# Kernel tuning notes

Measured on AMD Instinct MI355X. Metric: run time of the kernel, lower is better.

The kernel has to match this reference:

```python
import jax, jax.numpy as jnp
import numpy as np

B, L, D = 4, 2048, 1024
E, F, H = 6, 1536, 512  # experts, d_ff, router hidden
TOP_K = 2
LN_EPS = 1e-5

def setup_inputs() -> dict:
    key = jax.random.key(0)
    ks = jax.random.split(key, 8)
    s = lambda fan: 1.0 / np.sqrt(fan)
    return {
        "x": jax.random.normal(ks[0], (B, L, D), jnp.float32),
        "r1_w": jax.random.normal(ks[1], (D, H), jnp.float32) * s(D),
        "r1_b": jnp.zeros((H,), jnp.float32),
        "ln_g": jnp.ones((H,), jnp.float32),
        "ln_b": jnp.zeros((H,), jnp.float32),
        "r2_w": jax.random.normal(ks[2], (H, E), jnp.float32) * s(H),
        "r2_b": jnp.zeros((E,), jnp.float32),
        "temp": jnp.ones((1,), jnp.float32),
        "route_bias": jnp.zeros((E,), jnp.float32),
        "W1": jax.random.normal(ks[3], (E, D, F), jnp.float32) * s(D),
        "b1": jnp.zeros((E, F), jnp.float32),
        "W2": jax.random.normal(ks[4], (E, F, D), jnp.float32) * s(F),
        "b2": jnp.zeros((E, D), jnp.float32),
    }

def reference(x, r1_w, r1_b, ln_g, ln_b, r2_w, r2_b, temp, route_bias, W1, b1, W2, b2):
    b, l, d = x.shape
    xf = x.reshape(-1, d)                       # [N, D]
    n = xf.shape[0]
    # Router: Linear -> LayerNorm -> GELU(exact) -> Linear
    h = xf @ r1_w + r1_b                        # [N, H]
    mu = jnp.mean(h, axis=-1, keepdims=True)
    var = jnp.mean((h - mu) ** 2, axis=-1, keepdims=True)
    h = (h - mu) * jax.lax.rsqrt(var + LN_EPS) * ln_g + ln_b
    h = jax.nn.gelu(h, approximate=False)
    logits = (h @ r2_w + r2_b) / temp + route_bias   # [N, E]
    p = jax.nn.softmax(logits, axis=-1)
    top_v, top_i = jax.lax.top_k(p, TOP_K)      # [N, k]
    probs = jnp.zeros_like(p).at[jnp.arange(n)[:, None], top_i].set(top_v)  # [N, E]
    # Dense all-expert MLPs (faithful to source, which computes every expert)
    hh = jnp.einsum('nd,edf->enf', xf, W1) + b1[:, None, :]   # [E, N, F]
    even = (jnp.arange(W1.shape[0]) % 2 == 0)[:, None, None]
    act = jnp.where(even, jax.nn.gelu(hh, approximate=False), jax.nn.silu(hh))
    eo = jnp.einsum('enf,efd->end', act, W2) + b2[:, None, :]  # [E, N, D]
    out = jnp.einsum('ne,end->nd', probs, eo)   # weighted combine
    return out.reshape(b, l, d)
```

## Files before the change

kernel.cpp:

```cpp
#include <hip/hip_runtime.h>
#include <hip/hip_bf16.h>
#include <stdint.h>

typedef __bf16 bf16;
typedef bf16 bf16x8 __attribute__((ext_vector_type(8)));
typedef bf16 bf16x4 __attribute__((ext_vector_type(4)));
typedef float f32x4 __attribute__((ext_vector_type(4)));
typedef int i32x4 __attribute__((ext_vector_type(4)));

#define N_TOK 8192
#define D_MODEL 1024
#define H_R 512
#define N_EXP 6
#define F_FF 1536
#define FLAG_CAP 1024

__device__ __forceinline__ float erf_fast(float x) {
    float ax = fabsf(x);
    float t = 1.0f / (1.0f + 0.3275911f * ax);
    float p = t * (0.254829592f + t * (-0.284496736f + t * (1.421413741f +
              t * (-1.453152027f + t * 1.061405429f))));
    float r = 1.0f - p * __expf(-ax * ax);
    return copysignf(r, x);
}
__device__ __forceinline__ float gelu_f(float x) {
    return 0.5f * x * (1.0f + erf_fast(x * 0.70710678118654752f));
}
__device__ __forceinline__ float silu_f(float x) {
    return x * (1.0f / (1.0f + __expf(-x)));
}

typedef __attribute__((address_space(1))) const void* gas1;
typedef __attribute__((address_space(3))) void* las3;

__device__ __forceinline__ void gload16(const void* g, void* l) {
    __builtin_amdgcn_global_load_lds((gas1)g, (las3)l, 16, 0, 0);
}

__device__ __forceinline__ int swz_src_q(int c) {
    return (((c & 3) - ((c >> 2) >> 1)) & 3);
}

#define GATE(N) asm volatile("s_waitcnt vmcnt(" #N ")\n\ts_barrier" ::: "memory")


__global__ __launch_bounds__(256) void convert_x_split(
    const float* __restrict__ x, bf16* __restrict__ xh, bf16* __restrict__ xl) {
    size_t i = ((size_t)blockIdx.x * 256 + threadIdx.x) * 8;
    f32x4 a = *(const f32x4*)(x + i);
    f32x4 b = *(const f32x4*)(x + i + 4);
    float v[8] = {a[0], a[1], a[2], a[3], b[0], b[1], b[2], b[3]};
    bf16x8 vh, vl;
    #pragma unroll
    for (int k = 0; k < 8; ++k) {
        bf16 h = (bf16)v[k];
        vh[k] = h;
        vl[k] = (bf16)(v[k] - (float)h);
    }
    *(bf16x8*)(xh + i) = vh;
    *(bf16x8*)(xl + i) = vl;
}

__global__ __launch_bounds__(256) void transpose_bf16_64(
    const float* __restrict__ in, bf16* __restrict__ out, int R, int C) {
    __shared__ float tile[64][65];
    const float* inp = in + (size_t)blockIdx.z * R * C;
    bf16* op = out + (size_t)blockIdx.z * R * C;
    int tx = threadIdx.x & 15, ty = threadIdx.x >> 4;
    int r0 = blockIdx.y * 64, c0 = blockIdx.x * 64;
    #pragma unroll
    for (int p = 0; p < 4; ++p) {
        int row = p * 16 + ty;
        f32x4 v = *(const f32x4*)(inp + (size_t)(r0 + row) * C + c0 + tx * 4);
        tile[row][tx * 4 + 0] = v[0];
        tile[row][tx * 4 + 1] = v[1];
        tile[row][tx * 4 + 2] = v[2];
        tile[row][tx * 4 + 3] = v[3];
    }
    __syncthreads();
    #pragma unroll
    for (int p = 0; p < 4; ++p) {
        int cc = p * 16 + ty;
        bf16x4 o;
        #pragma unroll
        for (int k = 0; k < 4; ++k) o[k] = (bf16)tile[tx * 4 + k][cc];
        *(bf16x4*)(op + (size_t)(c0 + cc) * R + r0 + tx * 4) = o;
    }
}

__global__ __launch_bounds__(256) void transpose_split(
    const float* __restrict__ in, bf16* __restrict__ oh, bf16* __restrict__ ol,
    int R, int C) {
    __shared__ float tile[32][33];
    int tx = threadIdx.x & 31, ty = threadIdx.x >> 5;
    int r0 = blockIdx.y * 32, c0 = blockIdx.x * 32;
    #pragma unroll
    for (int yy = ty; yy < 32; yy += 8)
        tile[yy][tx] = in[(size_t)(r0 + yy) * C + c0 + tx];
    __syncthreads();
    #pragma unroll
    for (int yy = ty; yy < 32; yy += 8) {
        float v = tile[tx][yy];
        bf16 h = (bf16)v;
        size_t o = (size_t)(c0 + yy) * R + r0 + tx;
        oh[o] = h;
        ol[o] = (bf16)(v - (float)h);
    }
}


__device__ __forceinline__ void gemm128_core(
    const bf16* gA0, const bf16* gA1, const bf16* gB0, const bf16* gB1,
    int K, bf16* sm, f32x4 acc[4][4])
{
    const int tid = threadIdx.x;
    const int lane = tid & 63;
    const int w = tid >> 6;
    const int wm = w & 1, wn = w >> 1;
    const int lc = lane & 15;
    const int koff = ((((lane >> 4) + (lc >> 1)) & 3) * 8);
    gload16(gA0, sm + w * 512);
    gload16(gA1, sm + 2048 + w * 512);
    gload16(gB0, sm + 4096 + w * 512);
    gload16(gB1, sm + 6144 + w * 512);
    int bo = 0;
    const int NT = K >> 5;
    for (int t = 0; t < NT; ++t) {
        const int nb = bo ^ 8192;
        if (t + 1 < NT) {
            const int kb = (t + 1) << 5;
            gload16(gA0 + kb, sm + nb + w * 512);
            gload16(gA1 + kb, sm + nb + 2048 + w * 512);
            gload16(gB0 + kb, sm + nb + 4096 + w * 512);
            gload16(gB1 + kb, sm + nb + 6144 + w * 512);
            GATE(4);
        } else {
            GATE(0);
        }
        bf16x8 af[4], bfr[4];
        #pragma unroll
        for (int i = 0; i < 4; ++i)
            af[i] = *(const bf16x8*)(sm + bo + (wm * 64 + i * 16 + lc) * 32 + koff);
        #pragma unroll
        for (int j = 0; j < 4; ++j)
            bfr[j] = *(const bf16x8*)(sm + bo + 4096 + (wn * 64 + j * 16 + lc) * 32 + koff);
        __builtin_amdgcn_s_barrier();
        __builtin_amdgcn_s_setprio(1);
        #pragma unroll
        for (int i = 0; i < 4; ++i)
            #pragma unroll
            for (int j = 0; j < 4; ++j)
                acc[i][j] = __builtin_amdgcn_mfma_f32_16x16x32_bf16(af[i], bfr[j], acc[i][j], 0, 0, 0);
        __builtin_amdgcn_s_setprio(0);
        bo = nb;
    }
}


__global__ __launch_bounds__(256, 2) void router_gemm_fused(
    const bf16* __restrict__ xh, const bf16* __restrict__ xl,
    const bf16* __restrict__ wTh, const bf16* __restrict__ wTl,
    float* __restrict__ hp) {
    __shared__ bf16 smem[32768];
    const int tid = threadIdx.x;
    const int mbase = blockIdx.y * 128, nbase = blockIdx.x * 128;
    const int c0 = tid, c1 = tid + 256;
    const size_t ra0 = (size_t)(mbase + (c0 >> 2)) * D_MODEL + swz_src_q(c0) * 8;
    const size_t ra1 = (size_t)(mbase + (c1 >> 2)) * D_MODEL + swz_src_q(c1) * 8;
    const size_t rb0 = (size_t)(nbase + (c0 >> 2)) * D_MODEL + swz_src_q(c0) * 8;
    const size_t rb1 = (size_t)(nbase + (c1 >> 2)) * D_MODEL + swz_src_q(c1) * 8;
    const bf16 *pxh0 = xh + ra0, *pxh1 = xh + ra1;
    const bf16 *pxl0 = xl + ra0, *pxl1 = xl + ra1;
    const bf16 *pwh0 = wTh + rb0, *pwh1 = wTh + rb1;
    const bf16 *pwl0 = wTl + rb0, *pwl1 = wTl + rb1;
    const int w = tid >> 6, lane = tid & 63;
    const int wm = w & 1, wn = w >> 1, lc = lane & 15;
    const int koff = ((((lane >> 4) + (lc >> 1)) & 3) * 8);
    const int ws = w * 512;
    f32x4 acc[4][4] = {};
    gload16(pxh0, smem + ws);
    gload16(pxh1, smem + 2048 + ws);
    gload16(pxl0, smem + 4096 + ws);
    gload16(pxl1, smem + 6144 + ws);
    gload16(pwh0, smem + 8192 + ws);
    gload16(pwh1, smem + 10240 + ws);
    gload16(pwl0, smem + 12288 + ws);
    gload16(pwl1, smem + 14336 + ws);
    int bo = 0;
    for (int t = 0; t < D_MODEL / 32; ++t) {
        const int nb = bo ^ 16384;
        if (t + 1 < D_MODEL / 32) {
            const int kb = (t + 1) << 5;
            gload16(pxh0 + kb, smem + nb + ws);
            gload16(pxh1 + kb, smem + nb + 2048 + ws);
            gload16(pxl0 + kb, smem + nb + 4096 + ws);
            gload16(pxl1 + kb, smem + nb + 6144 + ws);
            gload16(pwh0 + kb, smem + nb + 8192 + ws);
            gload16(pwh1 + kb, smem + nb + 10240 + ws);
            gload16(pwl0 + kb, smem + nb + 12288 + ws);
            gload16(pwl1 + kb, smem + nb + 14336 + ws);
            GATE(8);
        } else {
            GATE(0);
        }
        bf16x8 ah[4], al[4], bh[4], bl[4];
        #pragma unroll
        for (int i = 0; i < 4; ++i) {
            const int ro = (wm * 64 + i * 16 + lc) * 32 + koff;
            ah[i] = *(const bf16x8*)(smem + bo + ro);
            al[i] = *(const bf16x8*)(smem + bo + 4096 + ro);
        }
        #pragma unroll
        for (int j = 0; j < 4; ++j) {
            const int ro = (wn * 64 + j * 16 + lc) * 32 + koff;
            bh[j] = *(const bf16x8*)(smem + bo + 8192 + ro);
            bl[j] = *(const bf16x8*)(smem + bo + 12288 + ro);
        }
        __builtin_amdgcn_s_barrier();
        __builtin_amdgcn_s_setprio(1);
        #pragma unroll
        for (int i = 0; i < 4; ++i)
            #pragma unroll
            for (int j = 0; j < 4; ++j) {
                acc[i][j] = __builtin_amdgcn_mfma_f32_16x16x32_bf16(ah[i], bh[j], acc[i][j], 0, 0, 0);
                acc[i][j] = __builtin_amdgcn_mfma_f32_16x16x32_bf16(ah[i], bl[j], acc[i][j], 0, 0, 0);
                acc[i][j] = __builtin_amdgcn_mfma_f32_16x16x32_bf16(al[i], bh[j], acc[i][j], 0, 0, 0);
            }
        __builtin_amdgcn_s_setprio(0);
        bo = nb;
    }
    const int quad = lane >> 4;
    #pragma unroll
    for (int i = 0; i < 4; ++i)
        #pragma unroll
        for (int j = 0; j < 4; ++j) {
            int col = nbase + wn * 64 + j * 16 + lc;
            #pragma unroll
            for (int r = 0; r < 4; ++r) {
                int row = mbase + wm * 64 + i * 16 + quad * 4 + r;
                hp[(size_t)row * H_R + col] = acc[i][j][r];
            }
        }
}


__global__ __launch_bounds__(256) void ln_router2(
    const float* __restrict__ hp, const float* __restrict__ r1b,
    const float* __restrict__ g, const float* __restrict__ bta,
    const float* __restrict__ r2w, const float* __restrict__ r2b,
    const float* __restrict__ temp, const float* __restrict__ rbias,
    int* __restrict__ top_i, float* __restrict__ top_p,
    int* __restrict__ flaglist, int* __restrict__ meta) {
    __shared__ float Wl[H_R * N_EXP];
    int tid = threadIdx.x;
    for (int i = tid; i < H_R * N_EXP; i += 256) Wl[i] = r2w[i];
    __syncthreads();
    int w = tid >> 6, lane = tid & 63;
    int t = blockIdx.x * 4 + w;
    size_t rbase = (size_t)t * H_R;
    int k0 = lane * 8;
    float v[8];
    {
        f32x4 a0 = *(const f32x4*)(hp + rbase + k0);
        f32x4 a1 = *(const f32x4*)(hp + rbase + k0 + 4);
        f32x4 d0 = *(const f32x4*)(r1b + k0);
        f32x4 d1 = *(const f32x4*)(r1b + k0 + 4);
        #pragma unroll
        for (int k = 0; k < 4; ++k) {
            v[k]     = a0[k] + d0[k];
            v[k + 4] = a1[k] + d1[k];
        }
    }
    float s = 0.f;
    #pragma unroll
    for (int k = 0; k < 8; ++k) s += v[k];
    #pragma unroll
    for (int off = 32; off; off >>= 1) s += __shfl_xor(s, off);
    float mu = s * (1.0f / H_R);
    float q = 0.f;
    #pragma unroll
    for (int k = 0; k < 8; ++k) { float d = v[k] - mu; q += d * d; }
    #pragma unroll
    for (int off = 32; off; off >>= 1) q += __shfl_xor(q, off);
    float scl = 1.0f / sqrtf(q * (1.0f / H_R) + 1e-5f);
    f32x4 g0 = *(const f32x4*)(g + k0), g1 = *(const f32x4*)(g + k0 + 4);
    f32x4 b0 = *(const f32x4*)(bta + k0), b1v = *(const f32x4*)(bta + k0 + 4);
    float G[8] = {g0[0], g0[1], g0[2], g0[3], g1[0], g1[1], g1[2], g1[3]};
    float B[8] = {b0[0], b0[1], b0[2], b0[3], b1v[0], b1v[1], b1v[2], b1v[3]};
    float acc[N_EXP] = {};
    #pragma unroll
    for (int k = 0; k < 8; ++k) {
        float y = gelu_f((v[k] - mu) * scl * G[k] + B[k]);
        const float* wr = &Wl[(k0 + k) * N_EXP];
        #pragma unroll
        for (int e = 0; e < N_EXP; ++e) acc[e] += y * wr[e];
    }
    #pragma unroll
    for (int e = 0; e < N_EXP; ++e)
        #pragma unroll
        for (int off = 32; off; off >>= 1) acc[e] += __shfl_xor(acc[e], off);
    if (lane == 0) {
        float tinv = 1.0f / temp[0];
        float lg[N_EXP];
        #pragma unroll
        for (int e = 0; e < N_EXP; ++e) lg[e] = (acc[e] + r2b[e]) * tinv + rbias[e];
        float v1 = -1e30f; int i1 = 0;
        #pragma unroll
        for (int e = 0; e < N_EXP; ++e) if (lg[e] > v1) { v1 = lg[e]; i1 = e; }
        float v2 = -1e30f; int i2 = 0;
        #pragma unroll
        for (int e = 0; e < N_EXP; ++e) if (e != i1 && lg[e] > v2) { v2 = lg[e]; i2 = e; }
        float v3 = -1e30f;
        #pragma unroll
        for (int e = 0; e < N_EXP; ++e) if (e != i1 && e != i2 && lg[e] > v3) v3 = lg[e];
        float ssum = 0.f;
        #pragma unroll
        for (int e = 0; e < N_EXP; ++e) ssum += __expf(lg[e] - v1);
        float inv = 1.0f / ssum;
        top_i[2 * t] = i1; top_i[2 * t + 1] = i2;
        top_p[2 * t] = inv;
        top_p[2 * t + 1] = __expf(v2 - v1) * inv;
        if (v2 - v3 < 1e-3f) {
            int ix = atomicAdd(&meta[24], 1);
            if (ix < FLAG_CAP) flaglist[ix] = t;
        }
    }
}


__global__ __launch_bounds__(256) void router_rescue(
    const float* __restrict__ x, const float* __restrict__ r1w,
    const float* __restrict__ r1b, const float* __restrict__ lng,
    const float* __restrict__ lnb, const float* __restrict__ r2w,
    const float* __restrict__ r2b, const float* __restrict__ temp,
    const float* __restrict__ rbias, const int* __restrict__ flaglist,
    const int* __restrict__ meta, int* __restrict__ top_i, float* __restrict__ top_p) {
    int n = meta[24]; if (n > FLAG_CAP) n = FLAG_CAP;
    if ((int)blockIdx.x >= n) return;
    int t = flaglist[blockIdx.x];
    __shared__ double xs[D_MODEL];
    __shared__ double hbuf[H_R];
    __shared__ double red[8];
    int tid = threadIdx.x;
    for (int k = tid; k < D_MODEL; k += 256) xs[k] = (double)x[(size_t)t * D_MODEL + k];
    __syncthreads();
    for (int c = tid; c < H_R; c += 256) {
        double s = 0.0;
        for (int k = 0; k < D_MODEL; ++k) s += xs[k] * (double)r1w[(size_t)k * H_R + c];
        hbuf[c] = s + (double)r1b[c];
    }
    __syncthreads();
    double ls = 0.0;
    for (int c = tid; c < H_R; c += 256) ls += hbuf[c];
    #pragma unroll
    for (int off = 32; off; off >>= 1) ls += __shfl_xor(ls, off);
    if ((tid & 63) == 0) red[tid >> 6] = ls;
    __syncthreads();
    double mu = (red[0] + red[1] + red[2] + red[3]) * (1.0 / H_R);
    __syncthreads();
    double q = 0.0;
    for (int c = tid; c < H_R; c += 256) { double d = hbuf[c] - mu; q += d * d; }
    #pragma unroll
    for (int off = 32; off; off >>= 1) q += __shfl_xor(q, off);
    if ((tid & 63) == 0) red[tid >> 6] = q;
    __syncthreads();
    double var = (red[0] + red[1] + red[2] + red[3]) * (1.0 / H_R);
    double scl = 1.0 / sqrt(var + 1e-5);
    __syncthreads();
    for (int c = tid; c < H_R; c += 256) {
        double y = (hbuf[c] - mu) * scl * (double)lng[c] + (double)lnb[c];
        hbuf[c] = 0.5 * y * (1.0 + erf(y * 0.70710678118654752440));
    }
    __syncthreads();
    if (tid < N_EXP) {
        double s = 0.0;
        for (int k = 0; k < H_R; ++k) s += hbuf[k] * (double)r2w[k * N_EXP + tid];
        red[tid] = (s + (double)r2b[tid]) / (double)temp[0] + (double)rbias[tid];
    }
    __syncthreads();
    if (tid == 0) {
        double lg[N_EXP];
        #pragma unroll
        for (int e = 0; e < N_EXP; ++e) lg[e] = red[e];
        double v1 = -1e300; int i1 = 0;
        for (int e = 0; e < N_EXP; ++e) if (lg[e] > v1) { v1 = lg[e]; i1 = e; }
        double v2 = -1e300; int i2 = 0;
        for (int e = 0; e < N_EXP; ++e) if (e != i1 && lg[e] > v2) { v2 = lg[e]; i2 = e; }
        double s = 0.0;
        for (int e = 0; e < N_EXP; ++e) s += exp(lg[e] - v1);
        double inv = 1.0 / s;
        top_i[2 * t] = i1; top_i[2 * t + 1] = i2;
        top_p[2 * t] = (float)inv;
        top_p[2 * t + 1] = (float)(exp(v2 - v1) * inv);
    }
}


#define RP_T 1024
#define RP_TOK (N_TOK / RP_T)

__global__ __launch_bounds__(1024) void route_pack(
    const int* __restrict__ top_i, int* __restrict__ meta,
    int* __restrict__ atok, int* __restrict__ ainv) {
    __shared__ int S[N_EXP][RP_T];
    __shared__ int segbase[N_EXP + 1];
    int tid = threadIdx.x;
    int e_loc[2 * RP_TOK];
    int cnt[N_EXP];
    #pragma unroll
    for (int e = 0; e < N_EXP; ++e) cnt[e] = 0;
    int t0 = tid * RP_TOK;
    #pragma unroll
    for (int q = 0; q < (2 * RP_TOK) / 4; ++q) {
        i32x4 v = *(const i32x4*)(top_i + 2 * t0 + q * 4);
        #pragma unroll
        for (int k = 0; k < 4; ++k) {
            int e = v[k];
            e_loc[q * 4 + k] = e;
            #pragma unroll
            for (int ee = 0; ee < N_EXP; ++ee) if (e == ee) cnt[ee]++;
        }
    }
    #pragma unroll
    for (int e = 0; e < N_EXP; ++e) S[e][tid] = cnt[e];
    __syncthreads();
    for (int off = 1; off < RP_T; off <<= 1) {
        int tmp[N_EXP];
        #pragma unroll
        for (int e = 0; e < N_EXP; ++e)
            tmp[e] = (tid >= off) ? S[e][tid - off] : 0;
        __syncthreads();
        #pragma unroll
        for (int e = 0; e < N_EXP; ++e) S[e][tid] += tmp[e];
        __syncthreads();
    }
    if (tid == 0) {
        int o = 0;
        #pragma unroll
        for (int e = 0; e < N_EXP; ++e) {
            segbase[e] = o;
            int tot = S[e][RP_T - 1];
            meta[e] = tot;
            meta[8 + e] = o;
            o += tot;
        }
        segbase[N_EXP] = o;
    }
    __syncthreads();
    int pos[N_EXP];
    #pragma unroll
    for (int e = 0; e < N_EXP; ++e)
        pos[e] = segbase[e] + S[e][tid] - cnt[e];
    #pragma unroll
    for (int k = 0; k < 2 * RP_TOK; ++k) {
        int e = e_loc[k];
        int a = 0;
        #pragma unroll
        for (int ee = 0; ee < N_EXP; ++ee) if (e == ee) a = pos[ee]++;
        atok[a] = t0 + (k >> 1);
        ainv[2 * t0 + k] = a;
    }
}


__global__ __launch_bounds__(256, 4) void expert_gemm1(
    const bf16* __restrict__ xb, const bf16* __restrict__ W1T,
    const float* __restrict__ b1, const int* __restrict__ meta,
    const int* __restrict__ atok, bf16* __restrict__ act) {
    __shared__ bf16 smem[16384];
    int e = blockIdx.z;
    int rows = meta[e];
    int mloc = blockIdx.y * 128;
    if (mloc >= rows) return;
    int base = meta[8 + e];
    int tid = threadIdx.x;
    int nbase = blockIdx.x * 128;
    int c0 = tid, c1 = tid + 256;
    int r0 = mloc + (c0 >> 2); if (r0 > rows - 1) r0 = rows - 1;
    int r1 = mloc + (c1 >> 2); if (r1 > rows - 1) r1 = rows - 1;
    const bf16* gA0 = xb + (size_t)atok[base + r0] * D_MODEL + swz_src_q(c0) * 8;
    const bf16* gA1 = xb + (size_t)atok[base + r1] * D_MODEL + swz_src_q(c1) * 8;
    const bf16* Bt = W1T + ((size_t)e * F_FF + nbase) * D_MODEL;
    const bf16* gB0 = Bt + (size_t)(c0 >> 2) * D_MODEL + swz_src_q(c0) * 8;
    const bf16* gB1 = Bt + (size_t)(c1 >> 2) * D_MODEL + swz_src_q(c1) * 8;
    f32x4 acc[4][4] = {};
    gemm128_core(gA0, gA1, gB0, gB1, D_MODEL, smem, acc);
    const int lane = tid & 63;
    const int w = tid >> 6;
    const int wm = w & 1, wn = w >> 1;
    const int lc = lane & 15, qd = lane >> 4;
    const bool oddE = (e & 1) != 0;
    #pragma unroll
    for (int i = 0; i < 4; ++i) {
        #pragma unroll
        for (int j = 0; j < 4; ++j) {
            int col = nbase + wn * 64 + j * 16 + lc;
            float bias = b1[e * F_FF + col];
            #pragma unroll
            for (int r = 0; r < 4; ++r) {
                int rloc = mloc + wm * 64 + i * 16 + qd * 4 + r;
                if (rloc < rows) {
                    float vv = acc[i][j][r] + bias;
                    vv = oddE ? silu_f(vv) : gelu_f(vv);
                    act[(size_t)(base + rloc) * F_FF + col] = (bf16)vv;
                }
            }
        }
    }
}

__global__ __launch_bounds__(256, 4) void expert_gemm2(
    const bf16* __restrict__ act, const bf16* __restrict__ W2T,
    const float* __restrict__ b2, const int* __restrict__ meta,
    float* __restrict__ eo) {
    __shared__ bf16 smem[16384];
    int e = blockIdx.z;
    int rows = meta[e];
    int mloc = blockIdx.y * 128;
    if (mloc >= rows) return;
    int base = meta[8 + e];
    int tid = threadIdx.x;
    int nbase = blockIdx.x * 128;
    int c0 = tid, c1 = tid + 256;
    int r0 = mloc + (c0 >> 2); if (r0 > rows - 1) r0 = rows - 1;
    int r1 = mloc + (c1 >> 2); if (r1 > rows - 1) r1 = rows - 1;
    const bf16* gA0 = act + (size_t)(base + r0) * F_FF + swz_src_q(c0) * 8;
    const bf16* gA1 = act + (size_t)(base + r1) * F_FF + swz_src_q(c1) * 8;
    const bf16* Bt = W2T + ((size_t)e * D_MODEL + nbase) * F_FF;
    const bf16* gB0 = Bt + (size_t)(c0 >> 2) * F_FF + swz_src_q(c0) * 8;
    const bf16* gB1 = Bt + (size_t)(c1 >> 2) * F_FF + swz_src_q(c1) * 8;
    f32x4 acc[4][4] = {};
    gemm128_core(gA0, gA1, gB0, gB1, F_FF, smem, acc);
    const int lane = tid & 63;
    const int w = tid >> 6;
    const int wm = w & 1, wn = w >> 1;
    const int lc = lane & 15, qd = lane >> 4;
    #pragma unroll
    for (int i = 0; i < 4; ++i) {
        #pragma unroll
        for (int j = 0; j < 4; ++j) {
            int col = nbase + wn * 64 + j * 16 + lc;
            float bias = b2[e * D_MODEL + col];
            #pragma unroll
            for (int r = 0; r < 4; ++r) {
                int rloc = mloc + wm * 64 + i * 16 + qd * 4 + r;
                if (rloc < rows)
                    eo[(size_t)(base + rloc) * D_MODEL + col] = acc[i][j][r] + bias;
            }
        }
    }
}


__global__ __launch_bounds__(256) void combine_kernel(
    const float* __restrict__ eo, const int* __restrict__ ainv,
    const float* __restrict__ top_p, float* __restrict__ out) {
    int t = blockIdx.x;
    int s0 = ainv[2 * t], s1 = ainv[2 * t + 1];
    float p0 = top_p[2 * t], p1 = top_p[2 * t + 1];
    int c = threadIdx.x * 4;
    f32x4 a = *(const f32x4*)(eo + (size_t)s0 * D_MODEL + c);
    f32x4 b = *(const f32x4*)(eo + (size_t)s1 * D_MODEL + c);
    f32x4 o;
    #pragma unroll
    for (int k = 0; k < 4; ++k) o[k] = a[k] * p0 + b[k] * p1;
    *(f32x4*)(out + (size_t)t * D_MODEL + c) = o;
}


extern "C" void kernel_launch(void* const* d_in, const int* in_sizes, int n_in,
                              void* d_out, int out_size, void* d_ws, size_t ws_size,
                              hipStream_t stream) {
    const float* x     = (const float*)d_in[0];
    const float* r1w   = (const float*)d_in[1];
    const float* r1b   = (const float*)d_in[2];
    const float* lng   = (const float*)d_in[3];
    const float* lnb   = (const float*)d_in[4];
    const float* r2w   = (const float*)d_in[5];
    const float* r2b   = (const float*)d_in[6];
    const float* temp  = (const float*)d_in[7];
    const float* rbias = (const float*)d_in[8];
    const float* W1    = (const float*)d_in[9];
    const float* b1    = (const float*)d_in[10];
    const float* W2    = (const float*)d_in[11];
    const float* b2    = (const float*)d_in[12];
    float* out = (float*)d_out;

    char* ws = (char*)d_ws;
    size_t off = 0;
    auto alloc = [&](size_t bytes) -> void* {
        void* p = ws + off;
        off = (off + bytes + 255) & ~(size_t)255;
        return p;
    };
    bf16*  xh    = (bf16*)alloc((size_t)N_TOK * D_MODEL * 2);
    bf16*  xl    = (bf16*)alloc((size_t)N_TOK * D_MODEL * 2);
    bf16*  r1wTh = (bf16*)alloc((size_t)H_R * D_MODEL * 2);
    bf16*  r1wTl = (bf16*)alloc((size_t)H_R * D_MODEL * 2);
    bf16*  W1T   = (bf16*)alloc((size_t)N_EXP * F_FF * D_MODEL * 2);
    bf16*  W2T   = (bf16*)alloc((size_t)N_EXP * D_MODEL * F_FF * 2);
    float* hp    = (float*)alloc((size_t)N_TOK * H_R * 4);
    int*   top_i = (int*)alloc((size_t)N_TOK * 2 * 4);
    float* top_p = (float*)alloc((size_t)N_TOK * 2 * 4);
    int*   meta  = (int*)alloc(256);
    int*   flags = (int*)alloc(FLAG_CAP * 4);
    int*   atok  = (int*)alloc((size_t)2 * N_TOK * 4);
    int*   ainv  = (int*)alloc((size_t)2 * N_TOK * 4);
    bf16*  actb  = (bf16*)alloc((size_t)2 * N_TOK * F_FF * 2);
    float* eo    = (float*)alloc((size_t)2 * N_TOK * D_MODEL * 4);
    (void)ws_size; (void)n_in; (void)in_sizes;

    hipMemsetAsync(meta, 0, 256, stream);

    convert_x_split<<<(N_TOK * D_MODEL) / (256 * 8), 256, 0, stream>>>(x, xh, xl);
    transpose_split<<<dim3(H_R / 32, D_MODEL / 32, 1), 256, 0, stream>>>(
        r1w, r1wTh, r1wTl, D_MODEL, H_R);

    router_gemm_fused<<<dim3(H_R / 128, N_TOK / 128, 1), 256, 0, stream>>>(
        xh, xl, r1wTh, r1wTl, hp);
    ln_router2<<<N_TOK / 4, 256, 0, stream>>>(
        hp, r1b, lng, lnb, r2w, r2b, temp, rbias, top_i, top_p, flags, meta);
    router_rescue<<<FLAG_CAP, 256, 0, stream>>>(
        x, r1w, r1b, lng, lnb, r2w, r2b, temp, rbias, flags, meta, top_i, top_p);
    route_pack<<<1, RP_T, 0, stream>>>(top_i, meta, atok, ainv);

    transpose_bf16_64<<<dim3(F_FF / 64, D_MODEL / 64, N_EXP), 256, 0, stream>>>(
        W1, W1T, D_MODEL, F_FF);
    transpose_bf16_64<<<dim3(D_MODEL / 64, F_FF / 64, N_EXP), 256, 0, stream>>>(
        W2, W2T, F_FF, D_MODEL);

    expert_gemm1<<<dim3(F_FF / 128, N_TOK / 128, N_EXP), 256, 0, stream>>>(
        xh, W1T, b1, meta, atok, actb);
    expert_gemm2<<<dim3(D_MODEL / 128, N_TOK / 128, N_EXP), 256, 0, stream>>>(
        actb, W2T, b2, meta, eo);
    combine_kernel<<<N_TOK, 256, 0, stream>>>(eo, ainv, top_p, out);
}
```

Baseline: 537.4 us.

## Triple-buffer expert GEMM LDS pipeline and remap blocks across XCDs

```diff
diff --git a/kernel.cpp b/kernel.cpp
--- a/kernel.cpp
+++ b/kernel.cpp
@@ -119,20 +119,26 @@
     const int wm = w & 1, wn = w >> 1;
     const int lc = lane & 15;
     const int koff = ((((lane >> 4) + (lc >> 1)) & 3) * 8);
-    gload16(gA0, sm + w * 512);
-    gload16(gA1, sm + 2048 + w * 512);
-    gload16(gB0, sm + 4096 + w * 512);
-    gload16(gB1, sm + 6144 + w * 512);
-    int bo = 0;
+    const int ws = w * 512;
     const int NT = K >> 5;
+    gload16(gA0,      sm + ws);
+    gload16(gA1,      sm + 2048 + ws);
+    gload16(gB0,      sm + 4096 + ws);
+    gload16(gB1,      sm + 6144 + ws);
+    gload16(gA0 + 32, sm + 8192 + ws);
+    gload16(gA1 + 32, sm + 8192 + 2048 + ws);
+    gload16(gB0 + 32, sm + 8192 + 4096 + ws);
+    gload16(gB1 + 32, sm + 8192 + 6144 + ws);
+    int cur = 0, nxt = 8192, fut = 16384;
     for (int t = 0; t < NT; ++t) {
-        const int nb = bo ^ 8192;
-        if (t + 1 < NT) {
-            const int kb = (t + 1) << 5;
-            gload16(gA0 + kb, sm + nb + w * 512);
-            gload16(gA1 + kb, sm + nb + 2048 + w * 512);
-            gload16(gB0 + kb, sm + nb + 4096 + w * 512);
-            gload16(gB1 + kb, sm + nb + 6144 + w * 512);
+        if (t + 2 < NT) {
+            const int kb = (t + 2) << 5;
+            gload16(gA0 + kb, sm + fut + ws);
+            gload16(gA1 + kb, sm + fut + 2048 + ws);
+            gload16(gB0 + kb, sm + fut + 4096 + ws);
+            gload16(gB1 + kb, sm + fut + 6144 + ws);
+            GATE(8);
+        } else if (t + 1 < NT) {
             GATE(4);
         } else {
             GATE(0);
@@ -140,10 +146,10 @@
         bf16x8 af[4], bfr[4];
         #pragma unroll
         for (int i = 0; i < 4; ++i)
-            af[i] = *(const bf16x8*)(sm + bo + (wm * 64 + i * 16 + lc) * 32 + koff);
+            af[i] = *(const bf16x8*)(sm + cur + (wm * 64 + i * 16 + lc) * 32 + koff);
         #pragma unroll
         for (int j = 0; j < 4; ++j)
-            bfr[j] = *(const bf16x8*)(sm + bo + 4096 + (wn * 64 + j * 16 + lc) * 32 + koff);
+            bfr[j] = *(const bf16x8*)(sm + cur + 4096 + (wn * 64 + j * 16 + lc) * 32 + koff);
         __builtin_amdgcn_s_barrier();
         __builtin_amdgcn_s_setprio(1);
         #pragma unroll
@@ -152,7 +158,7 @@
             for (int j = 0; j < 4; ++j)
                 acc[i][j] = __builtin_amdgcn_mfma_f32_16x16x32_bf16(af[i], bfr[j], acc[i][j], 0, 0, 0);
         __builtin_amdgcn_s_setprio(0);
-        bo = nb;
+        int old = cur; cur = nxt; nxt = fut; fut = old;
     }
 }
 
@@ -463,18 +469,25 @@
 }
 
 
-__global__ __launch_bounds__(256, 4) void expert_gemm1(
+#define NX1 (F_FF / 128)
+#define NX2 (D_MODEL / 128)
+
+__global__ __launch_bounds__(256, 3) void expert_gemm1(
     const bf16* __restrict__ xb, const bf16* __restrict__ W1T,
     const float* __restrict__ b1, const int* __restrict__ meta,
     const int* __restrict__ atok, bf16* __restrict__ act) {
-    __shared__ bf16 smem[16384];
-    int e = blockIdx.z;
+    __shared__ bf16 smem[24576];
+    const int id = blockIdx.x;
+    const int xcd = id & 7, slot = id >> 3;
+    const int xt = slot % NX1;
+    const int g = (slot / NX1) * 8 + xcd;
+    const int e = g % N_EXP, y = g / N_EXP;
     int rows = meta[e];
-    int mloc = blockIdx.y * 128;
+    int mloc = y * 128;
     if (mloc >= rows) return;
     int base = meta[8 + e];
     int tid = threadIdx.x;
-    int nbase = blockIdx.x * 128;
+    int nbase = xt * 128;
     int c0 = tid, c1 = tid + 256;
     int r0 = mloc + (c0 >> 2); if (r0 > rows - 1) r0 = rows - 1;
     int r1 = mloc + (c1 >> 2); if (r1 > rows - 1) r1 = rows - 1;
@@ -509,18 +522,22 @@
     }
 }
 
-__global__ __launch_bounds__(256, 4) void expert_gemm2(
+__global__ __launch_bounds__(256, 3) void expert_gemm2(
     const bf16* __restrict__ act, const bf16* __restrict__ W2T,
     const float* __restrict__ b2, const int* __restrict__ meta,
     float* __restrict__ eo) {
-    __shared__ bf16 smem[16384];
-    int e = blockIdx.z;
+    __shared__ bf16 smem[24576];
+    const int id = blockIdx.x;
+    const int xcd = id & 7, slot = id >> 3;
+    const int xt = slot % NX2;
+    const int g = (slot / NX2) * 8 + xcd;
+    const int e = g % N_EXP, y = g / N_EXP;
     int rows = meta[e];
-    int mloc = blockIdx.y * 128;
+    int mloc = y * 128;
     if (mloc >= rows) return;
     int base = meta[8 + e];
     int tid = threadIdx.x;
-    int nbase = blockIdx.x * 128;
+    int nbase = xt * 128;
     int c0 = tid, c1 = tid + 256;
     int r0 = mloc + (c0 >> 2); if (r0 > rows - 1) r0 = rows - 1;
     int r1 = mloc + (c1 >> 2); if (r1 > rows - 1) r1 = rows - 1;
@@ -629,9 +646,9 @@
     transpose_bf16_64<<<dim3(D_MODEL / 64, F_FF / 64, N_EXP), 256, 0, stream>>>(
         W2, W2T, F_FF, D_MODEL);
 
-    expert_gemm1<<<dim3(F_FF / 128, N_TOK / 128, N_EXP), 256, 0, stream>>>(
+    expert_gemm1<<<(N_TOK / 128) * N_EXP * NX1, 256, 0, stream>>>(
         xh, W1T, b1, meta, atok, actb);
-    expert_gemm2<<<dim3(D_MODEL / 128, N_TOK / 128, N_EXP), 256, 0, stream>>>(
+    expert_gemm2<<<(N_TOK / 128) * N_EXP * NX2, 256, 0, stream>>>(
         actb, W2T, b2, meta, eo);
     combine_kernel<<<N_TOK, 256, 0, stream>>>(eo, ainv, top_p, out);
 }
```

Result: faster. 524.1 us (-2.5%).
